# Optimization experiments

Measured on AMD Instinct MI355X. Metric: run time of the kernel, lower is better.

Reference implementation:

```python
import jax, jax.numpy as jnp
import numpy as np

B, S, D, H, DH, K, M = 2, 1024, 1024, 16, 64, 32, 8192
LN_EPS = 1e-5


def _ln(x, g, b):
    mu = jnp.mean(x, axis=-1, keepdims=True)
    var = jnp.var(x, axis=-1, keepdims=True)
    return (x - mu) * jax.lax.rsqrt(var + LN_EPS) * g + b


def _split_heads(t):  # [B,S,H*DH] -> [B,H,S,DH]
    return t.reshape(B, S, H, DH).transpose(0, 2, 1, 3)


def setup_inputs() -> dict:
    key = jax.random.key(0)
    ks = jax.random.split(key, 10)
    sd = 1.0 / np.sqrt(D)
    return {
        "x": jax.random.normal(ks[0], (B, S, D), jnp.float32),
        "mem_k_db": jax.random.normal(ks[1], (B, M, D), jnp.float32),
        "mem_v_db": jax.random.normal(ks[2], (B, M, D), jnp.float32),
        "g_val": jax.random.uniform(ks[3], (H,), jnp.float32),
        "ln1_g": jnp.ones((D,), jnp.float32),
        "ln1_b": jnp.zeros((D,), jnp.float32),
        "W_attn": jax.random.normal(ks[4], (D, 3 * D), jnp.float32) * sd,
        "b_attn": jnp.zeros((3 * D,), jnp.float32),
        "W_proj": jax.random.normal(ks[5], (D, D), jnp.float32) * sd,
        "b_proj": jnp.zeros((D,), jnp.float32),
        "ln2_g": jnp.ones((D,), jnp.float32),
        "ln2_b": jnp.zeros((D,), jnp.float32),
        "W_fc": jax.random.normal(ks[6], (D, 4 * D), jnp.float32) * sd,
        "b_fc": jnp.zeros((4 * D,), jnp.float32),
        "W_out": jax.random.normal(ks[7], (4 * D, D), jnp.float32) / np.sqrt(4 * D),
        "b_out": jnp.zeros((D,), jnp.float32),
    }


def reference(x, mem_k_db, mem_v_db, g_val, ln1_g, ln1_b, W_attn, b_attn,
              W_proj, b_proj, ln2_g, ln2_b, W_fc, b_fc, W_out, b_out):
    residual = x
    h = _ln(x, ln1_g, ln1_b)
    qkv = h @ W_attn + b_attn                       # [B,S,3D]
    q_f, k_f, v_f = jnp.split(qkv, 3, axis=-1)      # each [B,S,D]
    q = _split_heads(q_f)                           # [B,H,S,DH]
    k = _split_heads(k_f)
    v = _split_heads(v_f)

    # --- kNN memory search (non-per-head path): l2-normalized concat-head query ---
    sq = q_f / jnp.linalg.norm(q_f, axis=-1, keepdims=True).clip(1e-12)
    sims = jnp.einsum('bsd,bmd->bsm', sq, mem_k_db)          # [B,S,M]
    _, idx = jax.lax.top_k(sims, K)                          # [B,S,K]
    idx_e = idx[..., None]                                   # [B,S,K,1]
    mem_k = jnp.take_along_axis(mem_k_db[:, None], idx_e, axis=2)  # [B,S,K,D]
    mem_v = jnp.take_along_axis(mem_v_db[:, None], idx_e, axis=2)  # [B,S,K,D]
    # split memory into heads: [B,S,K,H*DH] -> [B,H,S,K,DH]
    mem_k = mem_k.reshape(B, S, K, H, DH).transpose(0, 3, 1, 2, 4)
    mem_v = mem_v.reshape(B, S, K, H, DH).transpose(0, 3, 1, 2, 4)

    inv_sqrt_dh = 1.0 / np.sqrt(DH)
    mem_w = jnp.einsum('bhid,bhijd->bhij', q, mem_k) * inv_sqrt_dh   # [B,H,S,K]

    std_w = jnp.einsum('bhid,bhjd->bhij', q, k) * inv_sqrt_dh        # [B,H,S,S]
    causal = jnp.tril(jnp.ones((S, S), bool))
    mask_val = jnp.finfo(std_w.dtype).min
    std_w = jnp.where(causal, std_w, mask_val)

    all_w = jax.nn.softmax(jnp.concatenate([mem_w, std_w], axis=-1), axis=-1)
    mem_attn, local_attn = all_w[..., :K], all_w[..., K:]

    local_out = jnp.einsum('bhij,bhjd->bhid', local_attn, v)
    mem_out = jnp.einsum('bhij,bhijd->bhid', mem_attn, mem_v)

    g = g_val.reshape(1, H, 1, 1)
    attn_out = (1.0 - g) * local_out + g * mem_out           # [B,H,S,DH]
    attn_out = attn_out.transpose(0, 2, 1, 3).reshape(B, S, D)
    attn_out = attn_out @ W_proj + b_proj

    h = attn_out + residual
    residual2 = h
    h = _ln(h, ln2_g, ln2_b)
    h = jax.nn.gelu(h @ W_fc + b_fc, approximate=True) @ W_out + b_out
    return residual2 + h
```

## Files before the change

### kernel.cpp

```cpp
#include <hip/hip_runtime.h>
#include <stdint.h>

#define DEV static __device__ __forceinline__

typedef __attribute__((ext_vector_type(8))) __bf16 bf16x8;
typedef __attribute__((ext_vector_type(4))) float f32x4;

DEV float bf2f(uint32_t u) {
  union { uint32_t i; float f; } v; v.i = u << 16; return v.f;
}
DEV uint16_t f2bf(float f) {
  union { float f; uint32_t i; } v; v.f = f;
  uint32_t x = v.i;
  return (uint16_t)((x + 0x7FFFu + ((x >> 16) & 1u)) >> 16);
}
DEV f32x4 mfma16(bf16x8 a, bf16x8 b, f32x4 c) {
  return __builtin_amdgcn_mfma_f32_16x16x32_bf16(a, b, c, 0, 0, 0);
}
DEV bf16x8 as_bf16x8(uint4 u) { return __builtin_bit_cast(bf16x8, u); }

DEV void gload16(const uint16_t* __restrict__ g, uint16_t* l) {
  __builtin_amdgcn_global_load_lds(
      (const __attribute__((address_space(1))) uint32_t*)g,
      (__attribute__((address_space(3))) uint32_t*)l, 16, 0, 0);
}

DEV float gelu_tanh(float x) {
  float x3 = x * x * x;
  float u = 0.7978845608028654f * (x + 0.044715f * x3);
  return 0.5f * x * (1.0f + tanhf(u));
}
DEV unsigned mono_key(float f) {
  union { float f; uint32_t u; } v; v.f = f;
  return (v.u & 0x80000000u) ? ~v.u : (v.u | 0x80000000u);
}

__global__ __launch_bounds__(256) void k_transpose_cast(
    const float* __restrict__ in, uint16_t* __restrict__ out,
    uint16_t* __restrict__ outlo, int R, int C) {
  __shared__ float tile[32][33];
  int c0 = blockIdx.x * 32, r0 = blockIdx.y * 32;
  int tx = threadIdx.x % 32, ty = threadIdx.x / 32;
  for (int i = 0; i < 32; i += 8)
    tile[ty + i][tx] = in[(size_t)(r0 + ty + i) * C + c0 + tx];
  __syncthreads();
  for (int i = 0; i < 32; i += 8) {
    float v = tile[tx][ty + i];
    uint16_t hi = f2bf(v);
    out[(size_t)(c0 + ty + i) * R + r0 + tx] = hi;
    if (outlo)
      outlo[(size_t)(c0 + ty + i) * R + r0 + tx] = f2bf(v - bf2f(hi));
  }
}

__global__ __launch_bounds__(256) void k_cast_bf16(
    const float* __restrict__ in, uint16_t* __restrict__ out, long n) {
  long i = ((long)blockIdx.x * 256 + threadIdx.x) * 4;
  if (i >= n) return;
  float4 v = *(const float4*)(in + i);
  uint2 pk;
  pk.x = (uint32_t)f2bf(v.x) | ((uint32_t)f2bf(v.y) << 16);
  pk.y = (uint32_t)f2bf(v.z) | ((uint32_t)f2bf(v.w) << 16);
  *(uint2*)(out + i) = pk;
}

__global__ __launch_bounds__(256) void k_layernorm(
    const float* __restrict__ x, const float* __restrict__ g,
    const float* __restrict__ bb, uint16_t* __restrict__ out,
    uint16_t* __restrict__ outlo) {
  int row = blockIdx.x;
  const float* xr = x + (size_t)row * 1024;
  int c = threadIdx.x * 4;
  float4 v = *(const float4*)(xr + c);
  float s = v.x + v.y + v.z + v.w;
  float s2 = v.x * v.x + v.y * v.y + v.z * v.z + v.w * v.w;
  for (int off = 32; off; off >>= 1) {
    s += __shfl_down(s, off, 64);
    s2 += __shfl_down(s2, off, 64);
  }
  __shared__ float ps[4], qs[4];
  int lane = threadIdx.x & 63, wv = threadIdx.x >> 6;
  if (!lane) { ps[wv] = s; qs[wv] = s2; }
  __syncthreads();
  float S = ps[0] + ps[1] + ps[2] + ps[3];
  float S2 = qs[0] + qs[1] + qs[2] + qs[3];
  float mu = S * (1.f / 1024.f);
  float var = S2 * (1.f / 1024.f) - mu * mu;
  float rinv = rsqrtf(var + 1e-5f);
  const float* vv = (const float*)&v;
  uint16_t o[4], ol[4];
#pragma unroll
  for (int j = 0; j < 4; j++) {
    float y = (vv[j] - mu) * rinv * g[c + j] + bb[c + j];
    o[j] = f2bf(y);
    ol[j] = f2bf(y - bf2f(o[j]));
  }
  uint2 pk;
  pk.x = (uint32_t)o[0] | ((uint32_t)o[1] << 16);
  pk.y = (uint32_t)o[2] | ((uint32_t)o[3] << 16);
  *(uint2*)(out + (size_t)row * 1024 + c) = pk;
  if (outlo) {
    pk.x = (uint32_t)ol[0] | ((uint32_t)ol[1] << 16);
    pk.y = (uint32_t)ol[2] | ((uint32_t)ol[3] << 16);
    *(uint2*)(outlo + (size_t)row * 1024 + c) = pk;
  }
}

template <int EPI>
__global__ __launch_bounds__(256) void k_gemm2(
    const uint16_t* __restrict__ A, int lda,
    const uint16_t* __restrict__ Bt, int ldb,
    void* __restrict__ Cout, int ldc,
    const float* __restrict__ bias,
    const float* __restrict__ resid,
    int Kc) {
  const int m0 = blockIdx.y * 64, n0 = blockIdx.x * 128;
  const int kt0 = (EPI & 16) ? blockIdx.z * Kc : 0;
  __shared__ __align__(16) uint16_t As[64 * 32];
  __shared__ __align__(16) uint16_t Bs[128 * 32];
  const int t = threadIdx.x, l = t & 63, w = t >> 6;
  const int lg = l >> 4, lr = l & 15;

  const int rA = w * 16 + (l >> 2);
  const uint16_t* pa = A + (size_t)(m0 + rA) * lda + kt0 + (((l & 3) ^ ((rA >> 1) & 3)) * 8);
  uint16_t* la = As + w * 512;
  const int rB0 = w * 16 + (l >> 2), rB1 = rB0 + 64;
  const uint16_t* pb0 = Bt + (size_t)(n0 + rB0) * ldb + kt0 + (((l & 3) ^ ((rB0 >> 1) & 3)) * 8);
  const uint16_t* pb1 = Bt + (size_t)(n0 + rB1) * ldb + kt0 + (((l & 3) ^ ((rB1 >> 1) & 3)) * 8);
  uint16_t* lb0 = Bs + w * 512;
  uint16_t* lb1 = Bs + 2048 + w * 512;

  int offA[4], offB[2];
#pragma unroll
  for (int i = 0; i < 4; i++) {
    int row = i * 16 + lr;
    offA[i] = ((row * 4 + lg) ^ ((row >> 1) & 3)) * 8;
  }
#pragma unroll
  for (int j = 0; j < 2; j++) {
    int row = w * 32 + j * 16 + lr;
    offB[j] = ((row * 4 + lg) ^ ((row >> 1) & 3)) * 8;
  }

  f32x4 acc[4][2] = {};
  for (int kt = 0; kt < Kc; kt += 32) {
    __syncthreads();
    gload16(pa, la);
    gload16(pb0, lb0);
    gload16(pb1, lb1);
    pa += 32; pb0 += 32; pb1 += 32;
    __syncthreads();
    bf16x8 af[4], bfr[2];
#pragma unroll
    for (int i = 0; i < 4; i++) af[i] = as_bf16x8(*(const uint4*)(As + offA[i]));
#pragma unroll
    for (int j = 0; j < 2; j++) bfr[j] = as_bf16x8(*(const uint4*)(Bs + offB[j]));
#pragma unroll
    for (int i = 0; i < 4; i++)
#pragma unroll
      for (int j = 0; j < 2; j++)
        acc[i][j] = mfma16(af[i], bfr[j], acc[i][j]);
  }
  const size_t zoff = (EPI & 16) ? (size_t)blockIdx.z * gridDim.y * 64 * ldc : 0;
#pragma unroll
  for (int i = 0; i < 4; i++)
#pragma unroll
    for (int j = 0; j < 2; j++)
#pragma unroll
      for (int r = 0; r < 4; r++) {
        int row = m0 + i * 16 + lg * 4 + r;
        int col = n0 + w * 32 + j * 16 + lr;
        float v = acc[i][j][r];
        if constexpr (EPI & 16) {
          ((float*)Cout)[zoff + (size_t)row * ldc + col] = v;
        } else {
          if constexpr (EPI & 1) v += bias[col];
          if constexpr (EPI & 4) v = gelu_tanh(v);
          if constexpr (EPI & 2) v += resid[(size_t)row * ldc + col];
          if constexpr (EPI & 8)
            ((uint16_t*)Cout)[(size_t)row * ldc + col] = f2bf(v);
          else
            ((float*)Cout)[(size_t)row * ldc + col] = v;
        }
      }
}

__global__ __launch_bounds__(256) void k_gemm_split2(
    const uint16_t* __restrict__ Ah, const uint16_t* __restrict__ Al, int lda,
    const uint16_t* __restrict__ Bh, const uint16_t* __restrict__ Bl, int ldb,
    uint16_t* __restrict__ Ch, uint16_t* __restrict__ Cl, int ldc,
    const float* __restrict__ bias, int Kd) {
  const int m0 = blockIdx.y * 64, n0 = blockIdx.x * 128;
  __shared__ __align__(16) uint16_t Ahs[64 * 32];
  __shared__ __align__(16) uint16_t Als[64 * 32];
  __shared__ __align__(16) uint16_t Bhs[128 * 32];
  __shared__ __align__(16) uint16_t Bls[128 * 32];
  const int t = threadIdx.x, l = t & 63, w = t >> 6;
  const int lg = l >> 4, lr = l & 15;

  const int rA = w * 16 + (l >> 2);
  const size_t aoff = (size_t)(m0 + rA) * lda + (((l & 3) ^ ((rA >> 1) & 3)) * 8);
  const uint16_t* pah = Ah + aoff;
  const uint16_t* pal = Al + aoff;
  uint16_t* lah = Ahs + w * 512;
  uint16_t* lal = Als + w * 512;
  const int rB0 = w * 16 + (l >> 2), rB1 = rB0 + 64;
  const size_t boff0 = (size_t)(n0 + rB0) * ldb + (((l & 3) ^ ((rB0 >> 1) & 3)) * 8);
  const size_t boff1 = (size_t)(n0 + rB1) * ldb + (((l & 3) ^ ((rB1 >> 1) & 3)) * 8);
  const uint16_t* pbh0 = Bh + boff0;
  const uint16_t* pbh1 = Bh + boff1;
  const uint16_t* pbl0 = Bl + boff0;
  const uint16_t* pbl1 = Bl + boff1;
  uint16_t* lbh0 = Bhs + w * 512;
  uint16_t* lbh1 = Bhs + 2048 + w * 512;
  uint16_t* lbl0 = Bls + w * 512;
  uint16_t* lbl1 = Bls + 2048 + w * 512;

  int offA[4], offB[2];
#pragma unroll
  for (int i = 0; i < 4; i++) {
    int row = i * 16 + lr;
    offA[i] = ((row * 4 + lg) ^ ((row >> 1) & 3)) * 8;
  }
#pragma unroll
  for (int j = 0; j < 2; j++) {
    int row = w * 32 + j * 16 + lr;
    offB[j] = ((row * 4 + lg) ^ ((row >> 1) & 3)) * 8;
  }

  f32x4 acc[4][2] = {};
  for (int kt = 0; kt < Kd; kt += 32) {
    __syncthreads();
    gload16(pah, lah); gload16(pal, lal);
    gload16(pbh0, lbh0); gload16(pbh1, lbh1);
    gload16(pbl0, lbl0); gload16(pbl1, lbl1);
    pah += 32; pal += 32; pbh0 += 32; pbh1 += 32; pbl0 += 32; pbl1 += 32;
    __syncthreads();
    bf16x8 ah[4], al[4], bh[2], bl[2];
#pragma unroll
    for (int i = 0; i < 4; i++) {
      ah[i] = as_bf16x8(*(const uint4*)(Ahs + offA[i]));
      al[i] = as_bf16x8(*(const uint4*)(Als + offA[i]));
    }
#pragma unroll
    for (int j = 0; j < 2; j++) {
      bh[j] = as_bf16x8(*(const uint4*)(Bhs + offB[j]));
      bl[j] = as_bf16x8(*(const uint4*)(Bls + offB[j]));
    }
#pragma unroll
    for (int i = 0; i < 4; i++)
#pragma unroll
      for (int j = 0; j < 2; j++) {
        acc[i][j] = mfma16(ah[i], bh[j], acc[i][j]);
        acc[i][j] = mfma16(ah[i], bl[j], acc[i][j]);
        acc[i][j] = mfma16(al[i], bh[j], acc[i][j]);
      }
  }
#pragma unroll
  for (int i = 0; i < 4; i++)
#pragma unroll
    for (int j = 0; j < 2; j++)
#pragma unroll
      for (int r = 0; r < 4; r++) {
        int row = m0 + i * 16 + lg * 4 + r;
        int col = n0 + w * 32 + j * 16 + lr;
        float v = acc[i][j][r] + bias[col];
        uint16_t hi = f2bf(v);
        Ch[(size_t)row * ldc + col] = hi;
        Cl[(size_t)row * ldc + col] = f2bf(v - bf2f(hi));
      }
}

template <int NP>
__global__ __launch_bounds__(256) void k_merge(
    const float* __restrict__ parts, const float* __restrict__ bias,
    const float* __restrict__ resid, float* __restrict__ out) {
  int row = blockIdx.x, c = threadIdx.x * 4;
  size_t off = (size_t)row * 1024 + c;
  float4 s = *(const float4*)(resid + off);
  float4 bv = *(const float4*)(bias + c);
  s.x += bv.x; s.y += bv.y; s.z += bv.z; s.w += bv.w;
#pragma unroll
  for (int z = 0; z < NP; z++) {
    float4 pv = *(const float4*)(parts + (size_t)z * 2048 * 1024 + off);
    s.x += pv.x; s.y += pv.y; s.z += pv.z; s.w += pv.w;
  }
  *(float4*)(out + off) = s;
}

__global__ __launch_bounds__(256) void k_topk2(
    const float* __restrict__ sims,
    const uint16_t* __restrict__ qkvh,
    const uint16_t* __restrict__ qkvl,
    const float* __restrict__ memk,
    int* __restrict__ idx_out,
    float* __restrict__ mlogh) {
  int row = blockIdx.x;
  int t = threadIdx.x;
  const float* s = sims + (size_t)row * 8192;
  unsigned key[32];
#pragma unroll
  for (int k = 0; k < 8; k++) {
    float4 v = *(const float4*)(s + t * 4 + k * 1024);
    key[k * 4 + 0] = mono_key(v.x);
    key[k * 4 + 1] = mono_key(v.y);
    key[k * 4 + 2] = mono_key(v.z);
    key[k * 4 + 3] = mono_key(v.w);
  }
  __shared__ int partial[4];
  __shared__ int cnt_s;
  __shared__ int sidx[40];
  __shared__ float qs[1024];
  __shared__ float hval[40][16];
  int lane = t & 63, wv = t >> 6;
  unsigned lo = 0u, hi = 0xFFFFFFFFu;
  for (int it = 0; it < 32; ++it) {
    unsigned mid = lo + ((hi - lo) >> 1);
    int c = 0;
#pragma unroll
    for (int i = 0; i < 32; i++) c += (key[i] > mid) ? 1 : 0;
    for (int off = 32; off; off >>= 1) c += __shfl_down(c, off, 64);
    if (!lane) partial[wv] = c;
    __syncthreads();
    int tot = partial[0] + partial[1] + partial[2] + partial[3];
    __syncthreads();
    if (tot >= 40) lo = mid + 1; else hi = mid;
  }
  unsigned T = lo;
  if (t == 0) cnt_s = 0;
  __syncthreads();
#pragma unroll
  for (int i = 0; i < 32; i++)
    if (key[i] > T) {
      int p = atomicAdd(&cnt_s, 1);
      if (p < 40) sidx[p] = t * 4 + (i >> 2) * 1024 + (i & 3);
    }
  __syncthreads();
#pragma unroll
  for (int i = 0; i < 32; i++)
    if (key[i] == T) {
      int p = atomicAdd(&cnt_s, 1);
      if (p < 40) sidx[p] = t * 4 + (i >> 2) * 1024 + (i & 3);
    }
  {
    int c4 = t * 4;
    const uint16_t* qh = qkvh + (size_t)row * 3072;
    const uint16_t* ql = qkvl + (size_t)row * 3072;
    uint2 uh = *(const uint2*)(qh + c4);
    uint2 ul = *(const uint2*)(ql + c4);
    qs[c4 + 0] = bf2f(uh.x & 0xFFFF) + bf2f(ul.x & 0xFFFF);
    qs[c4 + 1] = bf2f(uh.x >> 16) + bf2f(ul.x >> 16);
    qs[c4 + 2] = bf2f(uh.y & 0xFFFF) + bf2f(ul.y & 0xFFFF);
    qs[c4 + 3] = bf2f(uh.y >> 16) + bf2f(ul.y >> 16);
  }
  __syncthreads();
  {
    float4 qreg[4];
#pragma unroll
    for (int i = 0; i < 4; i++) qreg[i] = *(const float4*)(qs + i * 256 + lane * 4);
    for (int cc = 0; cc < 10; ++cc) {
      int c = wv * 10 + cc;
      const float* kp = memk + (size_t)sidx[c] * 1024;
#pragma unroll
      for (int i = 0; i < 4; ++i) {
        float4 kv = *(const float4*)(kp + i * 256 + lane * 4);
        float pband = kv.x * qreg[i].x + kv.y * qreg[i].y +
                      kv.z * qreg[i].z + kv.w * qreg[i].w;
        pband += __shfl_xor(pband, 1, 64);
        pband += __shfl_xor(pband, 2, 64);
        pband += __shfl_xor(pband, 4, 64);
        pband += __shfl_xor(pband, 8, 64);
        if ((lane & 15) == 0) hval[c][i * 4 + (lane >> 4)] = pband;
      }
    }
  }
  __syncthreads();
  if (wv == 0) {
    float full = 0.f;
    if (t < 40) {
#pragma unroll
      for (int i = 0; i < 16; i++) full += hval[t][i];
    }
    unsigned k2 = (t < 40) ? mono_key(full) : 0u;
    unsigned lo2 = 0u, hi2 = 0xFFFFFFFFu;
    for (int it = 0; it < 32; ++it) {
      unsigned mid = lo2 + ((hi2 - lo2) >> 1);
      int c = __popcll(__ballot(k2 > mid));
      if (c >= 32) lo2 = mid + 1; else hi2 = mid;
    }
    unsigned T2 = lo2;
    unsigned long long m1 = __ballot(k2 > T2);
    unsigned long long m2 = __ballot(k2 == T2);
    int n1 = __popcll(m1);
    unsigned long long lt = ((unsigned long long)1 << t) - 1;
    int pos = 99;
    if (k2 > T2) pos = __popcll(m1 & lt);
    else if (k2 == T2 && t < 40) pos = n1 + __popcll(m2 & lt);
    if (pos < 32) {
      idx_out[(size_t)row * 32 + pos] = sidx[t];
#pragma unroll
      for (int i = 0; i < 16; i++)
        mlogh[((size_t)row * 32 + pos) * 16 + i] = hval[t][i] * 0.125f;
    }
  }
}

__global__ __launch_bounds__(256) void k_flash(
    const uint16_t* __restrict__ qkvh,
    const uint16_t* __restrict__ qkvl,
    float* __restrict__ pacc,
    float* __restrict__ pm,
    float* __restrict__ pl) {
  const int qt = blockIdx.x, chk = blockIdx.y, bh = blockIdx.z;
  const int cbase = chk * 256;
  if (cbase >= (qt + 1) * 64) return;
  const int b = bh >> 4, h = bh & 15;
  const int t = threadIdx.x, lane = t & 63, w = t >> 6;
  const int lg = lane >> 4, lr = lane & 15;
  const int q0 = qt * 64 + w * 16;
  const size_t rowb = (size_t)b * 1024;
  __shared__ __align__(16) uint16_t Kh[2048];
  __shared__ __align__(16) uint16_t Kl[2048];
  __shared__ __align__(16) uint16_t Vs[2048];
  __shared__ __align__(16) uint16_t Pl[4][16][40];

  bf16x8 qh[2], qlo[2];
  {
    const uint16_t* qph = qkvh + (rowb + q0 + lr) * 3072 + h * 64;
    const uint16_t* qpl = qkvl + (rowb + q0 + lr) * 3072 + h * 64;
    qh[0] = as_bf16x8(*(const uint4*)(qph + lg * 8));
    qh[1] = as_bf16x8(*(const uint4*)(qph + 32 + lg * 8));
    qlo[0] = as_bf16x8(*(const uint4*)(qpl + lg * 8));
    qlo[1] = as_bf16x8(*(const uint4*)(qpl + 32 + lg * 8));
  }
  f32x4 acc[4] = {};
  float mrow[4], lrowv[4];
#pragma unroll
  for (int r = 0; r < 4; r++) { mrow[r] = -1e30f; lrowv[r] = 0.f; }

  const int lim = min(cbase + 256, q0 + 16);
  const int blim = min(cbase + 256, (qt + 1) * 64);

  const int sr = t >> 3, sc = t & 7;
  const int scs = sc ^ (sr & 7);
  const uint16_t* gkh = qkvh + (rowb + sr) * 3072 + 1024 + h * 64 + scs * 8;
  const uint16_t* gkl = qkvl + (rowb + sr) * 3072 + 1024 + h * 64 + scs * 8;
  const uint16_t* gv  = qkvh + (rowb + sr) * 3072 + 2048 + h * 64 + scs * 8;
  uint16_t* lkh = Kh + w * 512;
  uint16_t* lkl = Kl + w * 512;
  uint16_t* lv  = Vs + w * 512;

  for (int c0 = cbase; c0 < blim; c0 += 32) {
    const size_t so = (size_t)c0 * 3072;
    gload16(gkh + so, lkh);
    gload16(gkl + so, lkl);
    gload16(gv + so, lv);
    __syncthreads();
    if (c0 < lim) {
      f32x4 sf[2];
#pragma unroll
      for (int n = 0; n < 2; n++) {
        const int row = n * 16 + lr;
        const int rb = row * 64;
        const int x0 = ((lg) ^ (row & 7)) * 8;
        const int x1 = ((4 + lg) ^ (row & 7)) * 8;
        bf16x8 kh0 = as_bf16x8(*(const uint4*)(Kh + rb + x0));
        bf16x8 kh1 = as_bf16x8(*(const uint4*)(Kh + rb + x1));
        bf16x8 kl0 = as_bf16x8(*(const uint4*)(Kl + rb + x0));
        bf16x8 kl1 = as_bf16x8(*(const uint4*)(Kl + rb + x1));
        f32x4 sz = {};
        sz = mfma16(qh[0], kh0, sz);
        sz = mfma16(qh[1], kh1, sz);
        sz = mfma16(qh[0], kl0, sz);
        sz = mfma16(qh[1], kl1, sz);
        sz = mfma16(qlo[0], kh0, sz);
        sz = mfma16(qlo[1], kh1, sz);
        sf[n] = sz;
      }
      float p0[4], p1[4], alpha[4];
#pragma unroll
      for (int r = 0; r < 4; r++) {
        int rowq = q0 + lg * 4 + r;
        int col0 = c0 + lr, col1 = c0 + 16 + lr;
        float s0 = sf[0][r] * 0.125f; if (col0 > rowq) s0 = -1e30f;
        float s1 = sf[1][r] * 0.125f; if (col1 > rowq) s1 = -1e30f;
        float mt = fmaxf(s0, s1);
        mt = fmaxf(mt, __shfl_xor(mt, 1, 64));
        mt = fmaxf(mt, __shfl_xor(mt, 2, 64));
        mt = fmaxf(mt, __shfl_xor(mt, 4, 64));
        mt = fmaxf(mt, __shfl_xor(mt, 8, 64));
        float mnew = fmaxf(mrow[r], mt);
        float a = __expf(mrow[r] - mnew);
        float e0 = __expf(s0 - mnew), e1 = __expf(s1 - mnew);
        float ss = e0 + e1;
        ss += __shfl_xor(ss, 1, 64);
        ss += __shfl_xor(ss, 2, 64);
        ss += __shfl_xor(ss, 4, 64);
        ss += __shfl_xor(ss, 8, 64);
        lrowv[r] = lrowv[r] * a + ss;
        mrow[r] = mnew;
        alpha[r] = a;
        p0[r] = e0; p1[r] = e1;
      }
#pragma unroll
      for (int nv = 0; nv < 4; nv++)
#pragma unroll
        for (int r = 0; r < 4; r++) acc[nv][r] *= alpha[r];
#pragma unroll
      for (int r = 0; r < 4; r++) {
        Pl[w][lg * 4 + r][lr] = f2bf(p0[r]);
        Pl[w][lg * 4 + r][16 + lr] = f2bf(p1[r]);
      }
      bf16x8 pa = as_bf16x8(*(const uint4*)&Pl[w][lr][lg * 8]);
#pragma unroll
      for (int nv = 0; nv < 4; nv++) {
        const int col = nv * 16 + lr;
        const int cc = col >> 3, cl = col & 7;
        uint32_t vv[8];
#pragma unroll
        for (int j = 0; j < 8; j++) {
          int row = lg * 8 + j;
          vv[j] = Vs[row * 64 + ((cc ^ (row & 7)) * 8 + cl)];
        }
        uint4 pk;
        pk.x = vv[0] | (vv[1] << 16);
        pk.y = vv[2] | (vv[3] << 16);
        pk.z = vv[4] | (vv[5] << 16);
        pk.w = vv[6] | (vv[7] << 16);
        acc[nv] = mfma16(pa, as_bf16x8(pk), acc[nv]);
      }
    }
    __syncthreads();
  }
  const size_t base = (size_t)(chk * 32 + bh) * 1024;
#pragma unroll
  for (int nv = 0; nv < 4; nv++)
#pragma unroll
    for (int r = 0; r < 4; r++) {
      int rowq = q0 + lg * 4 + r;
      pacc[(base + rowq) * 64 + nv * 16 + lr] = acc[nv][r];
    }
  if (lr == 0) {
#pragma unroll
    for (int r = 0; r < 4; r++) {
      int rowq = q0 + lg * 4 + r;
      pm[base + rowq] = mrow[r];
      pl[base + rowq] = lrowv[r];
    }
  }
}

__global__ __launch_bounds__(256) void k_memcombine(
    const float* __restrict__ mlogh,
    const float* __restrict__ memv,
    const int* __restrict__ idx,
    const float* __restrict__ pacc,
    const float* __restrict__ pm,
    const float* __restrict__ pl,
    const float* __restrict__ gval,
    uint16_t* __restrict__ attnout) {
  int row = blockIdx.x;
  int b = row >> 10, s = row & 1023;
  int qt = s >> 6;
  int nact = (qt >> 2) + 1;
  __shared__ int sidx[32];
  __shared__ float lg[16][32];
  __shared__ float sp[16][32];
  __shared__ float smx[16], ssum[16];
  __shared__ float scl[16][4], Ms[16], Ls[16];
  int t = threadIdx.x;
  if (t < 32) sidx[t] = idx[(size_t)row * 32 + t];
  {
    const float* mp = mlogh + (size_t)row * 512;
#pragma unroll
    for (int rep = 0; rep < 2; rep++) {
      int i = t + rep * 256;
      lg[i & 15][i >> 4] = mp[i];
    }
  }
  __syncthreads();
  if (t < 16) {
    float mx = -1e30f;
#pragma unroll
    for (int j = 0; j < 32; j++) mx = fmaxf(mx, lg[t][j]);
    float su = 0.f;
    for (int j = 0; j < 32; j++) {
      float e = __expf(lg[t][j] - mx);
      sp[t][j] = e; su += e;
    }
    smx[t] = mx; ssum[t] = su;
  } else if (t >= 64 && t < 80) {
    int hh = t - 64;
    float pmv[4];
    float M = -1e30f;
    for (int c = 0; c < nact; c++) {
      pmv[c] = pm[(size_t)(c * 32 + b * 16 + hh) * 1024 + s];
      M = fmaxf(M, pmv[c]);
    }
    float L = 0.f;
    for (int c = 0; c < nact; c++) {
      float e = __expf(pmv[c] - M);
      scl[hh][c] = e;
      L += e * pl[(size_t)(c * 32 + b * 16 + hh) * 1024 + s];
    }
    Ms[hh] = M; Ls[hh] = L;
  }
  __syncthreads();
#pragma unroll
  for (int cc = 0; cc < 4; cc++) {
    int col = t + cc * 256;
    int hh = col >> 6;
    float ma = 0.f;
#pragma unroll
    for (int j = 0; j < 32; j++)
      ma += sp[hh][j] * memv[((size_t)b * 8192 + sidx[j]) * 1024 + col];
    float la = 0.f;
    for (int c = 0; c < nact; c++)
      la += scl[hh][c] *
            pacc[((size_t)(c * 32 + b * 16 + hh) * 1024 + s) * 64 + (col & 63)];
    float ms = Ms[hh], ls = Ls[hh];
    float mm = smx[hh], lmm = ssum[hh];
    float Mx = fmaxf(ms, mm);
    float es = __expf(ms - Mx), em = __expf(mm - Mx);
    float L = es * ls + em * lmm;
    float gh = gval[hh];
    float o = ((1.f - gh) * es * la + gh * em * ma) / L;
    attnout[(size_t)row * 1024 + col] = f2bf(o);
  }
}

extern "C" void kernel_launch(void* const* d_in, const int* in_sizes, int n_in,
                              void* d_out, int out_size, void* d_ws, size_t ws_size,
                              hipStream_t stream) {
  (void)in_sizes; (void)n_in; (void)out_size; (void)ws_size;
  const float* x     = (const float*)d_in[0];
  const float* memkf = (const float*)d_in[1];
  const float* memvf = (const float*)d_in[2];
  const float* gval  = (const float*)d_in[3];
  const float* ln1g  = (const float*)d_in[4];
  const float* ln1b  = (const float*)d_in[5];
  const float* Wattn = (const float*)d_in[6];
  const float* battn = (const float*)d_in[7];
  const float* Wproj = (const float*)d_in[8];
  const float* bproj = (const float*)d_in[9];
  const float* ln2g  = (const float*)d_in[10];
  const float* ln2b  = (const float*)d_in[11];
  const float* Wfc   = (const float*)d_in[12];
  const float* bfc   = (const float*)d_in[13];
  const float* Wout  = (const float*)d_in[14];
  const float* bout  = (const float*)d_in[15];

  char* p = (char*)d_ws;
  auto alloc = [&](size_t bytes) -> char* {
    char* r = p;
    p += (bytes + 255) & ~(size_t)255;
    return r;
  };
  uint16_t* h_hi    = (uint16_t*)alloc(2048ull * 1024 * 2);
  uint16_t* h_lo    = (uint16_t*)alloc(2048ull * 1024 * 2);
  uint16_t* WattnTh = (uint16_t*)alloc(3072ull * 1024 * 2);
  uint16_t* WattnTl = (uint16_t*)alloc(3072ull * 1024 * 2);
  uint16_t* WprojT  = (uint16_t*)alloc(1024ull * 1024 * 2);
  uint16_t* WfcT    = (uint16_t*)alloc(4096ull * 1024 * 2);
  uint16_t* WoutT   = (uint16_t*)alloc(1024ull * 4096 * 2);
  uint16_t* memk_bf = (uint16_t*)alloc(2ull * 8192 * 1024 * 2);
  uint16_t* qkv_hi  = (uint16_t*)alloc(2048ull * 3072 * 2);
  uint16_t* qkv_lo  = (uint16_t*)alloc(2048ull * 3072 * 2);
  float*    sims    = (float*)alloc(1024ull * 8192 * 4);
  int*      idx     = (int*)alloc(2048ull * 32 * 4);
  float*    mlogh   = (float*)alloc(2048ull * 32 * 16 * 4);
  float*    pm      = (float*)alloc(4ull * 32 * 1024 * 4);
  float*    pl      = (float*)alloc(4ull * 32 * 1024 * 4);
  float*    h1      = (float*)alloc(2048ull * 1024 * 4);
  uint16_t* attn_bf = (uint16_t*)alloc(2048ull * 1024 * 2);
  uint16_t* h2_bf   = h_hi;
  float*    pacc    = sims;
  uint16_t* ffn1    = (uint16_t*)sims;
  float*    parts   = (float*)memk_bf;

  k_transpose_cast<<<dim3(96, 32), 256, 0, stream>>>(Wattn, WattnTh, WattnTl, 1024, 3072);
  k_transpose_cast<<<dim3(32, 32), 256, 0, stream>>>(Wproj, WprojT, nullptr, 1024, 1024);
  k_transpose_cast<<<dim3(128, 32), 256, 0, stream>>>(Wfc, WfcT, nullptr, 1024, 4096);
  k_transpose_cast<<<dim3(32, 128), 256, 0, stream>>>(Wout, WoutT, nullptr, 4096, 1024);
  k_cast_bf16<<<16384, 256, 0, stream>>>(memkf, memk_bf, 2l * 8192 * 1024);

  k_layernorm<<<2048, 256, 0, stream>>>(x, ln1g, ln1b, h_hi, h_lo);
  k_gemm_split2<<<dim3(24, 32), 256, 0, stream>>>(h_hi, h_lo, 1024, WattnTh, WattnTl, 1024,
                                                  qkv_hi, qkv_lo, 3072, battn, 1024);
  for (int z = 0; z < 2; ++z) {
    k_gemm2<0><<<dim3(64, 16), 256, 0, stream>>>(
        qkv_hi + (size_t)z * 1024 * 3072, 3072,
        memk_bf + (size_t)z * 8192 * 1024, 1024,
        sims, 8192, nullptr, nullptr, 1024);
    k_topk2<<<1024, 256, 0, stream>>>(
        sims,
        qkv_hi + (size_t)z * 1024 * 3072,
        qkv_lo + (size_t)z * 1024 * 3072,
        memkf + (size_t)z * 8192 * 1024,
        idx + (size_t)z * 1024 * 32,
        mlogh + (size_t)z * 1024 * 32 * 16);
  }
  k_flash<<<dim3(16, 4, 32), 256, 0, stream>>>(qkv_hi, qkv_lo, pacc, pm, pl);
  k_memcombine<<<2048, 256, 0, stream>>>(mlogh, memvf, idx, pacc, pm, pl, gval, attn_bf);
  k_gemm2<16><<<dim3(8, 32, 2), 256, 0, stream>>>(attn_bf, 1024, WprojT, 1024,
                                                  parts, 1024, nullptr, nullptr, 512);
  k_merge<2><<<2048, 256, 0, stream>>>(parts, bproj, x, h1);
  k_layernorm<<<2048, 256, 0, stream>>>(h1, ln2g, ln2b, h2_bf, nullptr);
  k_gemm2<13><<<dim3(32, 32), 256, 0, stream>>>(h2_bf, 1024, WfcT, 1024,
                                                ffn1, 4096, bfc, nullptr, 1024);
  k_gemm2<16><<<dim3(8, 32, 4), 256, 0, stream>>>(ffn1, 4096, WoutT, 4096,
                                                  parts, 1024, nullptr, nullptr, 1024);
  k_merge<4><<<2048, 256, 0, stream>>>(parts, bout, h1, (float*)d_out);
}
```

Baseline: 476.3 us.

## Double-buffer K/V tiles in flash kernel, reverse tile order, trim top-k syncs

The flash attention kernel now double-buffers its K-hi/K-lo/V shared-memory tiles, prefetching the next 32-column chunk while the current one is computed, so global loads overlap MFMA work. Query tiles are scheduled in reverse so the heaviest causal tiles launch first. The top-k binary search double-buffers its partial-count array to drop one barrier per iteration. Shared memory use doubles for the K/V tiles, and the prefetch relies on the single trailing barrier to avoid overwriting a buffer that is still being read.

```diff
diff --git a/kernel.cpp b/kernel.cpp
--- a/kernel.cpp
+++ b/kernel.cpp
@@ -307,7 +307,7 @@
     key[k * 4 + 2] = mono_key(v.z);
     key[k * 4 + 3] = mono_key(v.w);
   }
-  __shared__ int partial[4];
+  __shared__ int partial[2][4];
   __shared__ int cnt_s;
   __shared__ int sidx[40];
   __shared__ float qs[1024];
@@ -320,10 +320,10 @@
 #pragma unroll
     for (int i = 0; i < 32; i++) c += (key[i] > mid) ? 1 : 0;
     for (int off = 32; off; off >>= 1) c += __shfl_down(c, off, 64);
-    if (!lane) partial[wv] = c;
+    if (!lane) partial[it & 1][wv] = c;
     __syncthreads();
-    int tot = partial[0] + partial[1] + partial[2] + partial[3];
-    __syncthreads();
+    int tot = partial[it & 1][0] + partial[it & 1][1] +
+              partial[it & 1][2] + partial[it & 1][3];
     if (tot >= 40) lo = mid + 1; else hi = mid;
   }
   unsigned T = lo;
@@ -411,7 +411,8 @@
     float* __restrict__ pacc,
     float* __restrict__ pm,
     float* __restrict__ pl) {
-  const int qt = blockIdx.x, chk = blockIdx.y, bh = blockIdx.z;
+  const int qt = 15 - blockIdx.x;
+  const int chk = blockIdx.y, bh = blockIdx.z;
   const int cbase = chk * 256;
   if (cbase >= (qt + 1) * 64) return;
   const int b = bh >> 4, h = bh & 15;
@@ -419,9 +420,9 @@
   const int lg = lane >> 4, lr = lane & 15;
   const int q0 = qt * 64 + w * 16;
   const size_t rowb = (size_t)b * 1024;
-  __shared__ __align__(16) uint16_t Kh[2048];
-  __shared__ __align__(16) uint16_t Kl[2048];
-  __shared__ __align__(16) uint16_t Vs[2048];
+  __shared__ __align__(16) uint16_t Kh[2][2048];
+  __shared__ __align__(16) uint16_t Kl[2][2048];
+  __shared__ __align__(16) uint16_t Vs[2][2048];
   __shared__ __align__(16) uint16_t Pl[4][16][40];
 
   bf16x8 qh[2], qlo[2];
@@ -446,16 +447,23 @@
   const uint16_t* gkh = qkvh + (rowb + sr) * 3072 + 1024 + h * 64 + scs * 8;
   const uint16_t* gkl = qkvl + (rowb + sr) * 3072 + 1024 + h * 64 + scs * 8;
   const uint16_t* gv  = qkvh + (rowb + sr) * 3072 + 2048 + h * 64 + scs * 8;
-  uint16_t* lkh = Kh + w * 512;
-  uint16_t* lkl = Kl + w * 512;
-  uint16_t* lv  = Vs + w * 512;
-
+
+  {
+    const size_t so = (size_t)cbase * 3072;
+    gload16(gkh + so, Kh[0] + w * 512);
+    gload16(gkl + so, Kl[0] + w * 512);
+    gload16(gv + so, Vs[0] + w * 512);
+  }
+  __syncthreads();
+
+  int cur = 0;
   for (int c0 = cbase; c0 < blim; c0 += 32) {
-    const size_t so = (size_t)c0 * 3072;
-    gload16(gkh + so, lkh);
-    gload16(gkl + so, lkl);
-    gload16(gv + so, lv);
-    __syncthreads();
+    if (c0 + 32 < blim) {
+      const size_t so = (size_t)(c0 + 32) * 3072;
+      gload16(gkh + so, Kh[cur ^ 1] + w * 512);
+      gload16(gkl + so, Kl[cur ^ 1] + w * 512);
+      gload16(gv + so, Vs[cur ^ 1] + w * 512);
+    }
     if (c0 < lim) {
       f32x4 sf[2];
 #pragma unroll
@@ -464,10 +472,10 @@
         const int rb = row * 64;
         const int x0 = ((lg) ^ (row & 7)) * 8;
         const int x1 = ((4 + lg) ^ (row & 7)) * 8;
-        bf16x8 kh0 = as_bf16x8(*(const uint4*)(Kh + rb + x0));
-        bf16x8 kh1 = as_bf16x8(*(const uint4*)(Kh + rb + x1));
-        bf16x8 kl0 = as_bf16x8(*(const uint4*)(Kl + rb + x0));
-        bf16x8 kl1 = as_bf16x8(*(const uint4*)(Kl + rb + x1));
+        bf16x8 kh0 = as_bf16x8(*(const uint4*)(Kh[cur] + rb + x0));
+        bf16x8 kh1 = as_bf16x8(*(const uint4*)(Kh[cur] + rb + x1));
+        bf16x8 kl0 = as_bf16x8(*(const uint4*)(Kl[cur] + rb + x0));
+        bf16x8 kl1 = as_bf16x8(*(const uint4*)(Kl[cur] + rb + x1));
         f32x4 sz = {};
         sz = mfma16(qh[0], kh0, sz);
         sz = mfma16(qh[1], kh1, sz);
@@ -520,7 +528,7 @@
 #pragma unroll
         for (int j = 0; j < 8; j++) {
           int row = lg * 8 + j;
-          vv[j] = Vs[row * 64 + ((cc ^ (row & 7)) * 8 + cl)];
+          vv[j] = Vs[cur][row * 64 + ((cc ^ (row & 7)) * 8 + cl)];
         }
         uint4 pk;
         pk.x = vv[0] | (vv[1] << 16);
@@ -531,6 +539,7 @@
       }
     }
     __syncthreads();
+    cur ^= 1;
   }
   const size_t base = (size_t)(chk * 32 + bh) * 1024;
 #pragma unroll
```

Measured after the change: 479.5 us. Within noise of the previous version (+0.7%).

## Store similarity matrix in bf16 and batch both sequences into single launches

Applied to the files above, without the earlier changes.

The similarity GEMM now writes its output as bf16 instead of fp32. A new EPI flag offsets A, B and C per batch through blockIdx.z, so both batch elements go through one GEMM launch and one top-k launch instead of a host loop of two each. The top-k kernel reads eight bf16 keys per 16-byte load and decodes global row and batch from blockIdx. The goal is to halve the write and read traffic of the large sims buffer and cut launch count. In exchange, near-ties in the bf16-rounded similarities may change which 40 candidates are kept before the exact rescoring.

```diff
diff --git a/kernel.cpp b/kernel.cpp
--- a/kernel.cpp
+++ b/kernel.cpp
@@ -116,6 +116,10 @@
     int Kc) {
   const int m0 = blockIdx.y * 64, n0 = blockIdx.x * 128;
   const int kt0 = (EPI & 16) ? blockIdx.z * Kc : 0;
+  if constexpr (EPI & 32) {
+    A += (size_t)blockIdx.z * 1024 * 3072;
+    Bt += (size_t)blockIdx.z * 8192 * 1024;
+  }
   __shared__ __align__(16) uint16_t As[64 * 32];
   __shared__ __align__(16) uint16_t Bs[128 * 32];
   const int t = threadIdx.x, l = t & 63, w = t >> 6;
@@ -161,7 +165,8 @@
       for (int j = 0; j < 2; j++)
         acc[i][j] = mfma16(af[i], bfr[j], acc[i][j]);
   }
-  const size_t zoff = (EPI & 16) ? (size_t)blockIdx.z * gridDim.y * 64 * ldc : 0;
+  const size_t zoff = (EPI & 16) ? (size_t)blockIdx.z * gridDim.y * 64 * ldc
+                    : (EPI & 32) ? (size_t)blockIdx.z * 1024 * 8192 : 0;
 #pragma unroll
   for (int i = 0; i < 4; i++)
 #pragma unroll
@@ -178,7 +183,7 @@
           if constexpr (EPI & 4) v = gelu_tanh(v);
           if constexpr (EPI & 2) v += resid[(size_t)row * ldc + col];
           if constexpr (EPI & 8)
-            ((uint16_t*)Cout)[(size_t)row * ldc + col] = f2bf(v);
+            ((uint16_t*)Cout)[zoff + (size_t)row * ldc + col] = f2bf(v);
           else
             ((float*)Cout)[(size_t)row * ldc + col] = v;
         }
@@ -289,23 +294,24 @@
 }
 
 __global__ __launch_bounds__(256) void k_topk2(
-    const float* __restrict__ sims,
-    const uint16_t* __restrict__ qkvh,
-    const uint16_t* __restrict__ qkvl,
-    const float* __restrict__ memk,
+    const uint16_t* __restrict__ simsb,
+    const uint16_t* __restrict__ qkvh_b,
+    const uint16_t* __restrict__ qkvl_b,
+    const float* __restrict__ memk_b,
     int* __restrict__ idx_out,
     float* __restrict__ mlogh) {
-  int row = blockIdx.x;
+  int grow = blockIdx.x;
+  int z = grow >> 10;
   int t = threadIdx.x;
-  const float* s = sims + (size_t)row * 8192;
+  const uint16_t* s16 = simsb + (size_t)grow * 8192;
+  const float* memk = memk_b + (size_t)z * 8192 * 1024;
   unsigned key[32];
 #pragma unroll
-  for (int k = 0; k < 8; k++) {
-    float4 v = *(const float4*)(s + t * 4 + k * 1024);
-    key[k * 4 + 0] = mono_key(v.x);
-    key[k * 4 + 1] = mono_key(v.y);
-    key[k * 4 + 2] = mono_key(v.z);
-    key[k * 4 + 3] = mono_key(v.w);
+  for (int k = 0; k < 4; k++) {
+    uint4 u = *(const uint4*)(s16 + t * 8 + k * 2048);
+    const uint16_t* pu = (const uint16_t*)&u;
+#pragma unroll
+    for (int j = 0; j < 8; j++) key[k * 8 + j] = mono_key(bf2f(pu[j]));
   }
   __shared__ int partial[4];
   __shared__ int cnt_s;
@@ -333,19 +339,19 @@
   for (int i = 0; i < 32; i++)
     if (key[i] > T) {
       int p = atomicAdd(&cnt_s, 1);
-      if (p < 40) sidx[p] = t * 4 + (i >> 2) * 1024 + (i & 3);
+      if (p < 40) sidx[p] = t * 8 + (i >> 3) * 2048 + (i & 7);
     }
   __syncthreads();
 #pragma unroll
   for (int i = 0; i < 32; i++)
     if (key[i] == T) {
       int p = atomicAdd(&cnt_s, 1);
-      if (p < 40) sidx[p] = t * 4 + (i >> 2) * 1024 + (i & 3);
+      if (p < 40) sidx[p] = t * 8 + (i >> 3) * 2048 + (i & 7);
     }
   {
     int c4 = t * 4;
-    const uint16_t* qh = qkvh + (size_t)row * 3072;
-    const uint16_t* ql = qkvl + (size_t)row * 3072;
+    const uint16_t* qh = qkvh_b + (size_t)grow * 3072;
+    const uint16_t* ql = qkvl_b + (size_t)grow * 3072;
     uint2 uh = *(const uint2*)(qh + c4);
     uint2 ul = *(const uint2*)(ql + c4);
     qs[c4 + 0] = bf2f(uh.x & 0xFFFF) + bf2f(ul.x & 0xFFFF);
@@ -397,10 +403,10 @@
     if (k2 > T2) pos = __popcll(m1 & lt);
     else if (k2 == T2 && t < 40) pos = n1 + __popcll(m2 & lt);
     if (pos < 32) {
-      idx_out[(size_t)row * 32 + pos] = sidx[t];
+      idx_out[(size_t)grow * 32 + pos] = sidx[t];
 #pragma unroll
       for (int i = 0; i < 16; i++)
-        mlogh[((size_t)row * 32 + pos) * 16 + i] = hval[t][i] * 0.125f;
+        mlogh[((size_t)grow * 32 + pos) * 16 + i] = hval[t][i] * 0.125f;
     }
   }
 }
@@ -674,6 +680,7 @@
   float*    h1      = (float*)alloc(2048ull * 1024 * 4);
   uint16_t* attn_bf = (uint16_t*)alloc(2048ull * 1024 * 2);
   uint16_t* h2_bf   = h_hi;
+  uint16_t* simsb   = (uint16_t*)sims;
   float*    pacc    = sims;
   uint16_t* ffn1    = (uint16_t*)sims;
   float*    parts   = (float*)memk_bf;
@@ -687,19 +694,9 @@
   k_layernorm<<<2048, 256, 0, stream>>>(x, ln1g, ln1b, h_hi, h_lo);
   k_gemm_split2<<<dim3(24, 32), 256, 0, stream>>>(h_hi, h_lo, 1024, WattnTh, WattnTl, 1024,
                                                   qkv_hi, qkv_lo, 3072, battn, 1024);
-  for (int z = 0; z < 2; ++z) {
-    k_gemm2<0><<<dim3(64, 16), 256, 0, stream>>>(
-        qkv_hi + (size_t)z * 1024 * 3072, 3072,
-        memk_bf + (size_t)z * 8192 * 1024, 1024,
-        sims, 8192, nullptr, nullptr, 1024);
-    k_topk2<<<1024, 256, 0, stream>>>(
-        sims,
-        qkv_hi + (size_t)z * 1024 * 3072,
-        qkv_lo + (size_t)z * 1024 * 3072,
-        memkf + (size_t)z * 8192 * 1024,
-        idx + (size_t)z * 1024 * 32,
-        mlogh + (size_t)z * 1024 * 32 * 16);
-  }
+  k_gemm2<40><<<dim3(64, 16, 2), 256, 0, stream>>>(
+      qkv_hi, 3072, memk_bf, 1024, simsb, 8192, nullptr, nullptr, 1024);
+  k_topk2<<<2048, 256, 0, stream>>>(simsb, qkv_hi, qkv_lo, memkf, idx, mlogh);
   k_flash<<<dim3(16, 4, 32), 256, 0, stream>>>(qkv_hi, qkv_lo, pacc, pm, pl);
   k_memcombine<<<2048, 256, 0, stream>>>(mlogh, memvf, idx, pacc, pm, pl, gval, attn_bf);
   k_gemm2<16><<<dim3(8, 32, 2), 256, 0, stream>>>(attn_bf, 1024, WprojT, 1024,
```

Measured after the change: 445.9 us. 6.4% less time.
